# Performance work log

Measured on AMD Instinct MI355X. Metric: run time of the kernel, lower is better.

The kernel has to match this reference:

```python
import jax, jax.numpy as jnp
import numpy as np

B, L, N = 16, 512, 32          # batch, seq_length, feature_size
E = 128                        # embed_size == frequency_size (number_frequency=1)
EMB = 8                        # embedding_dim
FCH = 64                       # fc_hidden_dim
H = 256                        # hidden_size
PRE = 96                       # pre_length
LAMBDA = 0.01                  # sparsity_threshold
SCALE = 0.02                   # init_scale


def softshrink(v, lambd=LAMBDA):
    return jnp.where(v > lambd, v - lambd, jnp.where(v < -lambd, v + lambd, 0.0))


def setup_inputs() -> dict:
    key = jax.random.key(0)
    ks = jax.random.split(key, 16)
    f32 = jnp.float32
    return {
        "x": jax.random.normal(ks[0], (B, L, N), f32),
        "emb": jax.random.normal(ks[1], (1, E), f32),
        "w0": SCALE * jax.random.normal(ks[2], (2, E, E), f32),
        "b0": SCALE * jax.random.normal(ks[3], (2, E), f32),
        "w1": SCALE * jax.random.normal(ks[4], (2, E, E), f32),
        "b1": SCALE * jax.random.normal(ks[5], (2, E), f32),
        "w2": SCALE * jax.random.normal(ks[6], (2, E, E), f32),
        "b2": SCALE * jax.random.normal(ks[7], (2, E), f32),
        "emb10": jax.random.normal(ks[8], (L, EMB), f32),
        "fc1_w": jax.random.normal(ks[9], (FCH, E * EMB), f32) / np.sqrt(E * EMB),
        "fc1_b": jnp.zeros((FCH,), f32),
        "fc2_w": jax.random.normal(ks[10], (H, FCH), f32) / np.sqrt(FCH),
        "fc2_b": jnp.zeros((H,), f32),
        "fc3_w": jax.random.normal(ks[11], (PRE, H), f32) / np.sqrt(H),
        "fc3_b": jnp.zeros((PRE,), f32),
    }


def _diag(w):
    # einsum 'bli,ii->bli' multiplies by the DIAGONAL of w only
    return jnp.diagonal(w, axis1=-2, axis2=-1)


def reference(x, emb, w0, b0, w1, b1, w2, b2, emb10,
              fc1_w, fc1_b, fc2_w, fc2_b, fc3_w, fc3_b):
    Bb = x.shape[0]
    xt = jnp.transpose(x, (0, 2, 1)).reshape(Bb, -1)          # [B, N*L]
    tok = xt[:, :, None] * emb                                 # [B, N*L, E]
    xf = jnp.fft.rfft(tok, axis=1, norm="ortho")               # [B, N*L//2+1, E] complex
    bias = xf

    # --- fourierGC (faithful to the torch op ordering, incl. o_real reuse) ---
    relu = jax.nn.relu
    d00, d01 = _diag(w0[0]), _diag(w0[1])
    o_r = relu(xf.real * d00 - xf.imag * d01 + b0[0])
    o_i = relu(xf.imag * d00 + xf.real * d01 + b0[1])
    prev = softshrink(jnp.stack([o_r, o_i], axis=-1))

    # middle layer (num_layers=3 -> one): note o_i uses the UPDATED o_r, as in torch
    d10, d11 = _diag(w1[0]), _diag(w1[1])
    o_r_new = relu(o_r * d10 - o_i * d11 + b1[0])
    o_i = relu(o_i * d10 + o_r_new * d11 + b1[1])
    o_r = o_r_new
    prev = softshrink(jnp.stack([o_r, o_i], axis=-1)) + prev

    # last layer
    d20, d21 = _diag(w2[0]), _diag(w2[1])
    o_r_new = relu(o_r * d20 - o_i * d21 + b2[0])
    o_i = relu(o_i * d20 + o_r_new * d21 + b2[1])
    z = softshrink(jnp.stack([o_r_new, o_i], axis=-1)) + prev
    zc = jax.lax.complex(z[..., 0], z[..., 1])

    xf = zc + bias
    xt = jnp.fft.irfft(xf, n=N * L, axis=1, norm="ortho")      # [B, N*L, E]
    xt = xt.reshape(Bb, N, L, E)
    xt = jnp.transpose(xt, (0, 1, 3, 2))                        # [B, N, E, L]
    h = jnp.matmul(xt, emb10)                                   # [B, N, E, EMB]
    h = h.reshape(Bb, N, E * EMB)

    lrelu = lambda v: jax.nn.leaky_relu(v, 0.01)
    h = lrelu(h @ fc1_w.T + fc1_b)
    h = lrelu(h @ fc2_w.T + fc2_b)
    out = h @ fc3_w.T + fc3_b                                   # [B, N, PRE]
    return out[:, 0, :]                                         # target_idx = 0
```

## Files before the change

kernel.cpp:

```cpp
#include <hip/hip_runtime.h>
#include <math.h>

#define Bsz   16
#define Lseq  512
#define Nfeat 32
#define E     128
#define EMB   8
#define FCH   64
#define Hd    256
#define PRE   96
#define M     16384
#define MH    8193
#define LAMBDA 0.01f

#define OFF_G   0
#define OFF_CS  524288
#define OFF_P   655376

#define REV_M   6.103515625e-5f
#define REV_128 7.8125e-3f

__device__ __forceinline__ float sin_rev(float r) { return __builtin_amdgcn_sinf(r); }
__device__ __forceinline__ float cos_rev(float r) { return __builtin_amdgcn_cosf(r); }

__global__ __launch_bounds__(256, 4)
void k_prep(const float* __restrict__ x, const float* __restrict__ emb10,
            float* __restrict__ ws) {
  __shared__ __align__(16) float sbuf[4160];
  int bid = blockIdx.x, tid = threadIdx.x;
  {
    int b = bid >> 6, t1base = (bid & 63) << 1;
    int t1loc = tid >> 7, idx = tid & 127;
    {
      int t = (t1base + t1loc) + 128 * idx;
      int n = t >> 9, l = t & 511;
      sbuf[t1loc * 128 + idx] = x[b * (Lseq * Nfeat) + l * Nfeat + n];
    }
    __syncthreads();
    int f1 = idx, t1 = t1base + t1loc;
    float s1 = sin_rev((float)f1 * REV_128), c1 = cos_rev((float)f1 * REV_128);
    float c2 = c1 * c1 - s1 * s1, s2 = 2.f * s1 * c1;
    float cA = 1.f, sA = 0.f, cB = c1, sB = s1;
    float grA = 0.f, giA = 0.f, grB = 0.f, giB = 0.f;
    const float2* xc2 = (const float2*)(sbuf + t1loc * 128);
    #pragma unroll 8
    for (int h = 0; h < 64; ++h) {
      float2 xv = xc2[h];
      grA = fmaf(xv.x, cA, grA); giA = fmaf(xv.x, -sA, giA);
      grB = fmaf(xv.y, cB, grB); giB = fmaf(xv.y, -sB, giB);
      float cn = cA * c2 - sA * s2; sA = sA * c2 + cA * s2; cA = cn;
      cn = cB * c2 - sB * s2;       sB = sB * c2 + cB * s2; cB = cn;
    }
    float gr = grA + grB, gi = giA + giB;
    float rv = (float)(f1 * t1) * REV_M;
    float sb = sin_rev(rv), cb = cos_rev(rv);
    float grr = gr * cb + gi * sb;
    float gii = gi * cb - gr * sb;
    float* G = ws + OFF_G + ((b * 128 + f1) * 128 + t1) * 2;
    G[0] = grr; G[1] = gii;
  }
  __syncthreads();
  {
    for (int j = tid; j < Lseq * EMB; j += 256) {
      int t = j >> 3, m = j & 7;
      sbuf[m * 512 + t] = emb10[j];
    }
    __syncthreads();
    int floc = tid >> 5, tl = tid & 31;
    int f = bid * 8 + floc;
    float ca[EMB], sa[EMB];
    #pragma unroll
    for (int m = 0; m < EMB; ++m) { ca[m] = 0.f; sa[m] = 0.f; }
    #pragma unroll 4
    for (int it = 0; it < 16; ++it) {
      int t = tl + 32 * it;
      int k = (f * t) & (M - 1);
      float rv = (float)k * REV_M;
      float cc = cos_rev(rv), ss = sin_rev(rv);
      #pragma unroll
      for (int m = 0; m < EMB; ++m) {
        float ev = sbuf[m * 512 + t];
        ca[m] = fmaf(cc, ev, ca[m]);
        sa[m] = fmaf(ss, ev, sa[m]);
      }
    }
    #pragma unroll
    for (int off = 16; off >= 1; off >>= 1) {
      #pragma unroll
      for (int m = 0; m < EMB; ++m) {
        ca[m] += __shfl_xor(ca[m], off, 64);
        sa[m] += __shfl_xor(sa[m], off, 64);
      }
    }
    if (tl == 0) {
      float wf = (f == 0) ? (1.0f / 128.0f) : (2.0f / 128.0f);
      float* o = ws + OFF_CS + f * 16;
      #pragma unroll
      for (int m = 0; m < EMB; ++m) { o[m] = ca[m] * wf; o[8 + m] = sa[m] * wf; }
    }
    if (bid == 0 && tid < 64) {
      int m = tid & 7, g = tid >> 3;
      float p = 0.f;
      #pragma unroll 8
      for (int j = 0; j < 64; ++j) p += sbuf[m * 512 + g + 8 * j];
      p = (g & 1) ? -p : p;
      p += __shfl_xor(p, 8, 64);
      p += __shfl_xor(p, 16, 64);
      p += __shfl_xor(p, 32, 64);
      if (g == 0) {
        ws[OFF_CS + 8192 * 16 + m] = p * (1.0f / 128.0f);
        ws[OFF_CS + 8192 * 16 + 8 + m] = 0.f;
      }
    }
  }
}

__global__ __launch_bounds__(256, 4)
void k_gcf(const float* __restrict__ emb,
           const float* __restrict__ w0, const float* __restrict__ b0,
           const float* __restrict__ w1, const float* __restrict__ b1,
           const float* __restrict__ w2, const float* __restrict__ b2,
           float* __restrict__ ws) {
  __shared__ __align__(16) float2 Gs[4][128];
  __shared__ __align__(16) float2 Xs[257];
  __shared__ float red[E * EMB];
  int f1g = blockIdx.x, b = blockIdx.y, tid = threadIdx.x;
  int f1base = f1g * 4;
  ((float4*)Gs)[tid] =
      ((const float4*)(ws + OFF_G + (b * 128 + f1base) * 256))[tid];
  __syncthreads();
  {
    int f1loc = tid >> 6, f2 = tid & 63;
    float s1 = sin_rev((float)f2 * REV_128), c1 = cos_rev((float)f2 * REV_128);
    float c = 1.f, s = 0.f;
    float xr = 0.f, xi = 0.f;
    const float2* g = Gs[f1loc];
    #pragma unroll 8
    for (int t1 = 0; t1 < 128; ++t1) {
      float2 gv = g[t1];
      xr = fmaf(gv.x, c, xr); xr = fmaf(gv.y, s, xr);
      xi = fmaf(gv.y, c, xi); xi = fmaf(-gv.x, s, xi);
      float cn = c * c1 - s * s1; s = s * c1 + c * s1; c = cn;
    }
    Xs[f1loc * 64 + f2] = make_float2(xr, xi);
    if (f1base == 0 && tid < 64) {
      float2 g0 = Gs[0][tid * 2], g1 = Gs[0][tid * 2 + 1];
      float er = g0.x - g1.x, ei = g0.y - g1.y;
      #pragma unroll
      for (int off = 1; off <= 32; off <<= 1) {
        er += __shfl_xor(er, off, 64);
        ei += __shfl_xor(ei, off, 64);
      }
      if (tid == 0) Xs[256] = make_float2(er, ei);
    }
  }
  __syncthreads();
  int e = tid & 127, fh = tid >> 7;
  int nf = (f1base == 0) ? 257 : 256;
  float se  = emb[e] * (1.0f / 128.0f);
  float d00 = w0[e * 129], d01 = w0[E * E + e * 129];
  float c00 = b0[e],       c01 = b0[E + e];
  float d10 = w1[e * 129], d11 = w1[E * E + e * 129];
  float c10 = b1[e],       c11 = b1[E + e];
  float d20 = w2[e * 129], d21 = w2[E * E + e * 129];
  float c20 = b2[e],       c21 = b2[E + e];
  float acc[EMB];
  #pragma unroll
  for (int m = 0; m < EMB; ++m) acc[m] = 0.f;

  for (int i = fh; i < nf; i += 2) {
    int iu = __builtin_amdgcn_readfirstlane(i);
    int f = (iu == 256) ? 8192 : (f1base + (iu >> 6) + ((iu & 63) << 7));
    const float* cs = ws + OFF_CS + f * 16;
    float2 X = Xs[iu];
    float xr = X.x * se, xi = X.y * se;
    float or0 = fmaxf(fmaf(xr, d00, fmaf(-xi, d01, c00)), 0.f);
    float oi0 = fmaxf(fmaf(xi, d00, fmaf(xr, d01, c01)), 0.f);
    float pr = fmaxf(or0 - LAMBDA, 0.f), pi = fmaxf(oi0 - LAMBDA, 0.f);
    float or1 = fmaxf(fmaf(or0, d10, fmaf(-oi0, d11, c10)), 0.f);
    float oi1 = fmaxf(fmaf(oi0, d10, fmaf(or1, d11, c11)), 0.f);
    pr += fmaxf(or1 - LAMBDA, 0.f); pi += fmaxf(oi1 - LAMBDA, 0.f);
    float u2r = fmaf(or1, d20, fmaf(-oi1, d21, c20));
    float or2 = fmaxf(u2r, 0.f);
    float u2i = fmaf(oi1, d20, fmaf(or2, d21, c21));
    float zr = fmaxf(u2r - LAMBDA, 0.f) + pr;
    float zi = fmaxf(u2i - LAMBDA, 0.f) + pi;
    #pragma unroll
    for (int m = 0; m < EMB; ++m)
      acc[m] = fmaf(zr, cs[m], fmaf(-zi, cs[8 + m], acc[m]));
  }
  __syncthreads();
  if (fh == 1) {
    #pragma unroll
    for (int m = 0; m < EMB; ++m) red[e * EMB + m] = acc[m];
  }
  __syncthreads();
  if (fh == 0) {
    float* P = ws + OFF_P + (f1g * 16 + b) * (E * EMB) + e * EMB;
    #pragma unroll
    for (int m = 0; m < EMB; ++m) P[m] = acc[m] + red[e * EMB + m];
  }
}

__global__ __launch_bounds__(1024)
void k_fc(const float* __restrict__ x, const float* __restrict__ emb,
          const float* __restrict__ emb10,
          const float* __restrict__ fc1w, const float* __restrict__ fc1b,
          const float* __restrict__ fc2w, const float* __restrict__ fc2b,
          const float* __restrict__ fc3w, const float* __restrict__ fc3b,
          const float* __restrict__ ws, float* __restrict__ out) {
  int b = blockIdx.x;
  __shared__ float h0s[E * EMB];
  __shared__ float h1s[FCH];
  __shared__ float h2s[Hd];
  __shared__ float hxs[EMB];
  __shared__ float scratch[1024];
  int tid = threadIdx.x;
  int lane = tid & 63, w = tid >> 6;
  {
    int m = tid & 7, g = tid >> 3;
    float p = 0.f;
    #pragma unroll
    for (int l = g; l < Lseq; l += 128)
      p = fmaf(x[b * (Lseq * Nfeat) + l * Nfeat], emb10[l * EMB + m], p);
    scratch[tid] = p;
  }
  const float* P = ws + OFF_P + b * (E * EMB) + tid;
  float a = 0.f;
  #pragma unroll
  for (int c = 0; c < 32; ++c) a += P[c * (Bsz * E * EMB)];
  __syncthreads();
  if (tid < 8) {
    float s = 0.f;
    #pragma unroll 16
    for (int g = 0; g < 128; ++g) s += scratch[g * 8 + tid];
    hxs[tid] = s;
  }
  __syncthreads();
  h0s[tid] = a + emb[tid >> 3] * hxs[tid & 7];
  __syncthreads();
  #pragma unroll
  for (int oo = 0; oo < 4; ++oo) {
    int o = oo * 16 + w;
    const float* wr = fc1w + o * (E * EMB);
    float acc = 0.f;
    #pragma unroll
    for (int j = 0; j < 16; ++j) acc = fmaf(h0s[lane + 64 * j], wr[lane + 64 * j], acc);
    #pragma unroll
    for (int off = 32; off >= 1; off >>= 1) acc += __shfl_xor(acc, off, 64);
    if (lane == 0) { float v = acc + fc1b[o]; h1s[o] = v > 0.f ? v : 0.01f * v; }
  }
  __syncthreads();
  #pragma unroll
  for (int oo = 0; oo < 16; ++oo) {
    int o = oo * 16 + w;
    float acc = h1s[lane] * fc2w[o * FCH + lane];
    #pragma unroll
    for (int off = 32; off >= 1; off >>= 1) acc += __shfl_xor(acc, off, 64);
    if (lane == 0) { float v = acc + fc2b[o]; h2s[o] = v > 0.f ? v : 0.01f * v; }
  }
  __syncthreads();
  #pragma unroll
  for (int oo = 0; oo < 6; ++oo) {
    int o = oo * 16 + w;
    const float* wr = fc3w + o * Hd;
    float acc = 0.f;
    #pragma unroll
    for (int j = 0; j < 4; ++j) acc = fmaf(h2s[lane + 64 * j], wr[lane + 64 * j], acc);
    #pragma unroll
    for (int off = 32; off >= 1; off >>= 1) acc += __shfl_xor(acc, off, 64);
    if (lane == 0) out[b * PRE + o] = acc + fc3b[o];
  }
}

extern "C" void kernel_launch(void* const* d_in, const int* in_sizes, int n_in,
                              void* d_out, int out_size, void* d_ws, size_t ws_size,
                              hipStream_t stream) {
  const float* x     = (const float*)d_in[0];
  const float* emb   = (const float*)d_in[1];
  const float* w0    = (const float*)d_in[2];
  const float* b0    = (const float*)d_in[3];
  const float* w1    = (const float*)d_in[4];
  const float* b1    = (const float*)d_in[5];
  const float* w2    = (const float*)d_in[6];
  const float* b2    = (const float*)d_in[7];
  const float* emb10 = (const float*)d_in[8];
  const float* fc1w  = (const float*)d_in[9];
  const float* fc1b  = (const float*)d_in[10];
  const float* fc2w  = (const float*)d_in[11];
  const float* fc2b  = (const float*)d_in[12];
  const float* fc3w  = (const float*)d_in[13];
  const float* fc3b  = (const float*)d_in[14];
  float* ws  = (float*)d_ws;
  float* out = (float*)d_out;

  k_prep<<<dim3(1024), 256, 0, stream>>>(x, emb10, ws);
  k_gcf<<<dim3(32, Bsz), 256, 0, stream>>>(emb, w0, b0, w1, b1, w2, b2, ws);
  k_fc<<<dim3(Bsz), 1024, 0, stream>>>(x, emb, emb10, fc1w, fc1b, fc2w, fc2b,
                                       fc3w, fc3b, ws, out);
}
```

Measured before the change: 177.1 us.

## Widen k_gcf to 1024 threads, splitting DFT and frequency loops across more waves

Raises k_gcf from 256 to 1024 threads per block. The 128-point inner DFT is split into four 32-element chunks with a padded shared layout, and partial sums are combined with lane shuffles. The per-frequency loop now strides by 8 instead of 2, with a larger shared reduction at the end. The goal is to cut the per-thread serial loop length and raise occupancy on a grid of only 512 blocks. In exchange it adds shuffle and reduction overhead and uses more shared memory.

Result: faster. 148.4 us (-16.2%).

```diff
diff --git a/kernel.cpp b/kernel.cpp
--- a/kernel.cpp
+++ b/kernel.cpp
@@ -115,36 +115,47 @@
   }
 }
 
-__global__ __launch_bounds__(256, 4)
+__global__ __launch_bounds__(1024, 8)
 void k_gcf(const float* __restrict__ emb,
            const float* __restrict__ w0, const float* __restrict__ b0,
            const float* __restrict__ w1, const float* __restrict__ b1,
            const float* __restrict__ w2, const float* __restrict__ b2,
            float* __restrict__ ws) {
-  __shared__ __align__(16) float2 Gs[4][128];
+  __shared__ __align__(16) float2 Gs[4 * 132];
   __shared__ __align__(16) float2 Xs[257];
-  __shared__ float red[E * EMB];
+  __shared__ float red[7 * 1024];
   int f1g = blockIdx.x, b = blockIdx.y, tid = threadIdx.x;
   int f1base = f1g * 4;
-  ((float4*)Gs)[tid] =
-      ((const float4*)(ws + OFF_G + (b * 128 + f1base) * 256))[tid];
+  if (tid < 512) {
+    float2 v = ((const float2*)(ws + OFF_G + (b * 128 + f1base) * 256))[tid];
+    int f1loc = tid >> 7, t1 = tid & 127;
+    Gs[f1loc * 132 + (t1 >> 5) * 33 + (t1 & 31)] = v;
+  }
   __syncthreads();
   {
-    int f1loc = tid >> 6, f2 = tid & 63;
+    int w = tid >> 6, lane = tid & 63;
+    int f1loc = w >> 2;
+    int q = lane >> 4, f2 = ((w & 3) << 4) + (lane & 15);
+    int r = (f2 * q) & 3;
+    float c = (r == 0) ? 1.f : (r == 2) ? -1.f : 0.f;
+    float s = (r == 1) ? 1.f : (r == 3) ? -1.f : 0.f;
     float s1 = sin_rev((float)f2 * REV_128), c1 = cos_rev((float)f2 * REV_128);
-    float c = 1.f, s = 0.f;
     float xr = 0.f, xi = 0.f;
-    const float2* g = Gs[f1loc];
+    const float2* g = Gs + f1loc * 132 + q * 33;
     #pragma unroll 8
-    for (int t1 = 0; t1 < 128; ++t1) {
-      float2 gv = g[t1];
+    for (int k = 0; k < 32; ++k) {
+      float2 gv = g[k];
       xr = fmaf(gv.x, c, xr); xr = fmaf(gv.y, s, xr);
       xi = fmaf(gv.y, c, xi); xi = fmaf(-gv.x, s, xi);
       float cn = c * c1 - s * s1; s = s * c1 + c * s1; c = cn;
     }
-    Xs[f1loc * 64 + f2] = make_float2(xr, xi);
+    xr += __shfl_xor(xr, 16, 64); xi += __shfl_xor(xi, 16, 64);
+    xr += __shfl_xor(xr, 32, 64); xi += __shfl_xor(xi, 32, 64);
+    if (lane < 16) Xs[f1loc * 64 + f2] = make_float2(xr, xi);
     if (f1base == 0 && tid < 64) {
-      float2 g0 = Gs[0][tid * 2], g1 = Gs[0][tid * 2 + 1];
+      int t1v = tid * 2;
+      const float2* g0p = Gs + (t1v >> 5) * 33;
+      float2 g0 = g0p[t1v & 31], g1 = g0p[(t1v & 31) + 1];
       float er = g0.x - g1.x, ei = g0.y - g1.y;
       #pragma unroll
       for (int off = 1; off <= 32; off <<= 1) {
@@ -168,7 +179,7 @@
   #pragma unroll
   for (int m = 0; m < EMB; ++m) acc[m] = 0.f;
 
-  for (int i = fh; i < nf; i += 2) {
+  for (int i = fh; i < nf; i += 8) {
     int iu = __builtin_amdgcn_readfirstlane(i);
     int f = (iu == 256) ? 8192 : (f1base + (iu >> 6) + ((iu & 63) << 7));
     const float* cs = ws + OFF_CS + f * 16;
@@ -190,15 +201,19 @@
       acc[m] = fmaf(zr, cs[m], fmaf(-zi, cs[8 + m], acc[m]));
   }
   __syncthreads();
-  if (fh == 1) {
-    #pragma unroll
-    for (int m = 0; m < EMB; ++m) red[e * EMB + m] = acc[m];
+  if (fh > 0) {
+    #pragma unroll
+    for (int m = 0; m < EMB; ++m) red[(fh - 1) * 1024 + e * EMB + m] = acc[m];
   }
   __syncthreads();
   if (fh == 0) {
+    #pragma unroll
+    for (int j = 0; j < 7; ++j)
+      #pragma unroll
+      for (int m = 0; m < EMB; ++m) acc[m] += red[j * 1024 + e * EMB + m];
     float* P = ws + OFF_P + (f1g * 16 + b) * (E * EMB) + e * EMB;
     #pragma unroll
-    for (int m = 0; m < EMB; ++m) P[m] = acc[m] + red[e * EMB + m];
+    for (int m = 0; m < EMB; ++m) P[m] = acc[m];
   }
 }
 
@@ -295,7 +310,7 @@
   float* out = (float*)d_out;
 
   k_prep<<<dim3(1024), 256, 0, stream>>>(x, emb10, ws);
-  k_gcf<<<dim3(32, Bsz), 256, 0, stream>>>(emb, w0, b0, w1, b1, w2, b2, ws);
+  k_gcf<<<dim3(32, Bsz), 1024, 0, stream>>>(emb, w0, b0, w1, b1, w2, b2, ws);
   k_fc<<<dim3(Bsz), 1024, 0, stream>>>(x, emb, emb10, fc1w, fc1b, fc2w, fc2b,
                                        fc3w, fc3b, ws, out);
 }
```
